# Optimization experiments

Measured on AMD Instinct MI355X. Metric: run time of the kernel, lower is better.

The kernel has to match this reference:

```python
import jax, jax.numpy as jnp
import numpy as np

N_NODES = 100_000
N_EDGES = 1_600_000
DIM_IN = 256
ADD_TO_EDGE_SCORE = 0.5  # PyG EdgePooling default


def setup_inputs() -> dict:
    key = jax.random.key(0)
    k1, k2, k3 = jax.random.split(key, 3)
    x = jax.random.normal(k1, (N_NODES, DIM_IN), dtype=jnp.float32)
    edge_index = jax.random.randint(k2, (2, N_EDGES), 0, N_NODES, dtype=jnp.int32)
    batch = jnp.zeros((N_NODES,), dtype=jnp.int32)  # single graph
    W = jax.random.normal(k3, (2 * DIM_IN, 1), dtype=jnp.float32) / np.sqrt(2.0 * DIM_IN)
    b = jnp.zeros((1,), dtype=jnp.float32)
    return {"x": x, "edge_index": edge_index, "batch": batch, "W": W, "b": b}


def _segment_softmax(scores, seg, num_segments):
    m = jax.ops.segment_max(scores, seg, num_segments=num_segments)
    ex = jnp.exp(scores - m[seg])
    s = jax.ops.segment_sum(ex, seg, num_segments=num_segments)
    return ex / s[seg]


def _greedy_matching(rank, src, dst, num_nodes):
    """Maximal matching equivalent to sequential greedy over edges sorted by
    ascending rank (rank = position in descending-score argsort, a strict total
    order). Implemented as parallel locally-dominant matching rounds."""
    big = jnp.iinfo(jnp.int32).max

    def cond(state):
        alive, matched, chosen = state
        return jnp.any(alive)

    def body(state):
        alive, matched, chosen = state
        r = jnp.where(alive, rank, big)
        node_min = jnp.full((num_nodes,), big, dtype=jnp.int32)
        node_min = node_min.at[src].min(r)
        node_min = node_min.at[dst].min(r)
        # an alive edge is picked if it dominates all alive edges at both endpoints
        pick = alive & (rank == node_min[src]) & (rank == node_min[dst])
        matched = matched.at[jnp.where(pick, src, num_nodes)].set(True, mode='drop')
        matched = matched.at[jnp.where(pick, dst, num_nodes)].set(True, mode='drop')
        chosen = chosen | pick
        alive = alive & ~matched[src] & ~matched[dst]
        return alive, matched, chosen

    alive0 = jnp.ones_like(rank, dtype=bool)
    matched0 = jnp.zeros((num_nodes,), dtype=bool)
    chosen0 = jnp.zeros_like(alive0)
    _, matched, chosen = jax.lax.while_loop(cond, body, (alive0, matched0, chosen0))
    return chosen, matched


def reference(x, edge_index, batch, W, b):
    num_nodes, feat = x.shape
    num_edges = edge_index.shape[1]
    src, dst = edge_index[0], edge_index[1]

    # Linear([x_src || x_dst]) split to avoid materializing [E, 2F]
    s_src = x @ W[:feat, 0]   # [N]
    s_dst = x @ W[feat:, 0]   # [N]
    raw = s_src[src] + s_dst[dst] + b[0]            # [E]
    # dropout is identity in eval mode
    e = _segment_softmax(raw, dst, num_nodes) + ADD_TO_EDGE_SCORE  # [E]

    # rank: position of each edge in descending-score order
    order = jnp.argsort(-e)
    rank = jnp.zeros((num_edges,), dtype=jnp.int32).at[order].set(
        jnp.arange(num_edges, dtype=jnp.int32))

    chosen, matched = _greedy_matching(rank, src, dst, num_nodes)

    # cluster id of each chosen edge = its position among chosen edges in score order
    chosen_sorted = chosen[order]
    cid_sorted = jnp.cumsum(chosen_sorted.astype(jnp.int32)) - 1
    cid = jnp.zeros((num_edges,), dtype=jnp.int32).at[order].set(cid_sorted)
    num_matched = jnp.sum(chosen.astype(jnp.int32))

    # node -> cluster assignment; unmatched nodes get trailing singleton clusters
    cluster = jnp.zeros((num_nodes,), dtype=jnp.int32)
    cluster = cluster.at[jnp.where(chosen, src, num_nodes)].set(cid, mode='drop')
    cluster = cluster.at[jnp.where(chosen, dst, num_nodes)].set(cid, mode='drop')
    unm = num_matched + jnp.cumsum((~matched).astype(jnp.int32)) - 1
    cluster = jnp.where(matched, cluster, unm)
    num_clusters = num_matched + jnp.sum((~matched).astype(jnp.int32))

    # per-cluster score: chosen-edge scores for merged pairs, 1.0 for singletons
    new_edge_score = jnp.ones((num_nodes,), dtype=x.dtype)
    new_edge_score = new_edge_score.at[jnp.where(chosen, cid, num_nodes)].set(e, mode='drop')

    # scatter-merge node features (rows >= num_clusters are zero padding)
    new_x = jax.ops.segment_sum(x, cluster, num_segments=num_nodes)
    new_x = new_x * new_edge_score[:, None]

    new_edge_index = cluster[edge_index]  # remapped edges (coalesce/dedup omitted)
    new_batch = jnp.zeros((num_nodes,), dtype=batch.dtype).at[cluster].set(batch)

    return new_x, new_edge_index, new_batch, num_clusters
```

## Files before the change

kernel.cpp:

```cpp
#include <hip/hip_runtime.h>

typedef unsigned int u32;
typedef unsigned long long u64;
typedef unsigned char u8;

static constexpr int SORTN = 65536;
static constexpr int STILE = 2048;
static constexpr int NR    = 12;
static constexpr int NHEAVY= 3;
static constexpr int NXCD  = 8;

__device__ __forceinline__ u32 xccid() {
  u32 x;
  asm volatile("s_getreg_b32 %0, hwreg(HW_REG_XCC_ID)" : "=s"(x));
  return x & (NXCD - 1);
}

__device__ __forceinline__ void wmin64(u64* p, u64 v) {
  __hip_atomic_fetch_min(p, v, __ATOMIC_RELAXED, __HIP_MEMORY_SCOPE_WORKGROUP);
}
__device__ __forceinline__ void wmax32(u32* p, u32 v) {
  __hip_atomic_fetch_max(p, v, __ATOMIC_RELAXED, __HIP_MEMORY_SCOPE_WORKGROUP);
}
__device__ __forceinline__ void waddf64(double* p, double v) {
  __hip_atomic_fetch_add(p, v, __ATOMIC_RELAXED, __HIP_MEMORY_SCOPE_WORKGROUP);
}

__device__ __forceinline__ u32 ordf(float f) {
  u32 u = __float_as_uint(f);
  return (u & 0x80000000u) ? ~u : (u | 0x80000000u);
}
__device__ __forceinline__ float inv_ordf(u32 m) {
  return __uint_as_float((m & 0x80000000u) ? (m ^ 0x80000000u) : ~m);
}

__global__ __launch_bounds__(256)
void k_init(u32* m_ord, u32* m8, double* ssum, double* ss8, u8* matched,
            u64* node_min, u64* nm8, float* scoreC, ulonglong2* sortbuf,
            u32* fcnt, u32* scalars, int N, int E) {
  int i = blockIdx.x * blockDim.x + threadIdx.x;
  if (i < N) { m_ord[i] = 0u; ssum[i] = 0.0; matched[i] = 0; scoreC[i] = 1.0f; }
  if (i < 2 * N) node_min[i] = ~0ull;
  if (i < NXCD * N) { nm8[i] = ~0ull; m8[i] = 0u; ss8[i] = 0.0; }
  if (i < SORTN) sortbuf[i] = make_ulonglong2(~0ull, ~0ull);
  if (i < 256)   fcnt[i] = 0u;
  if (i < 16)    scalars[i] = 0u;
  if (i == 0)    fcnt[0] = (u32)E;
}

__global__ __launch_bounds__(256)
void k_dots(const float4* __restrict__ x4, const float4* __restrict__ W4,
            float* __restrict__ s_src, float* __restrict__ s_dst, int N) {
  int gt = blockIdx.x * blockDim.x + threadIdx.x;
  int w = gt >> 6, lane = gt & 63;
  if (w >= N) return;
  float4 xa = x4[(size_t)w * 64 + lane];
  float4 wa = W4[lane];
  float4 wb = W4[64 + lane];
  float pa = xa.x*wa.x + xa.y*wa.y + xa.z*wa.z + xa.w*wa.w;
  float pb = xa.x*wb.x + xa.y*wb.y + xa.z*wb.z + xa.w*wb.w;
  #pragma unroll
  for (int m = 32; m >= 1; m >>= 1) {
    pa += __shfl_xor(pa, m);
    pb += __shfl_xor(pb, m);
  }
  if (lane == 0) { s_src[w] = pa; s_dst[w] = pb; }
}

__global__ __launch_bounds__(256)
void k_max8(const int* __restrict__ src, const int* __restrict__ dst,
            const float* __restrict__ s_src, const float* __restrict__ s_dst,
            const float* __restrict__ bvec, u32* m8, int N, int E) {
  int e = blockIdx.x * blockDim.x + threadIdx.x;
  if (e >= E) return;
  u32* mW = m8 + (size_t)xccid() * N;
  int d = dst[e];
  float r = s_src[src[e]] + s_dst[d] + bvec[0];
  wmax32(&mW[d], ordf(r));
}

__global__ __launch_bounds__(256)
void k_maxmerge(const u32* __restrict__ m8, u32* __restrict__ m_ord, int N) {
  int v = blockIdx.x * 256 + threadIdx.x;
  if (v >= N) return;
  u32 m = 0u;
  #pragma unroll
  for (int x = 0; x < NXCD; x++) {
    u32 t = m8[(size_t)x * N + v];
    m = (t > m) ? t : m;
  }
  m_ord[v] = m;
}

__global__ __launch_bounds__(256)
void k_expsum8(const int* __restrict__ src, const int* __restrict__ dst,
               const float* __restrict__ s_src, const float* __restrict__ s_dst,
               const float* __restrict__ bvec, const u32* __restrict__ m_ord,
               double* ss8, int N, int E) {
  int e = blockIdx.x * blockDim.x + threadIdx.x;
  if (e >= E) return;
  double* sW = ss8 + (size_t)xccid() * N;
  int d = dst[e];
  float r = s_src[src[e]] + s_dst[d] + bvec[0];
  float ex = expf(r - inv_ordf(m_ord[d]));
  waddf64(&sW[d], (double)ex);
}

__global__ __launch_bounds__(256)
void k_ssmerge(const double* __restrict__ ss8, double* __restrict__ ssum, int N) {
  int v = blockIdx.x * 256 + threadIdx.x;
  if (v >= N) return;
  double s = 0.0;
  #pragma unroll
  for (int x = 0; x < NXCD; x++) s += ss8[(size_t)x * N + v];
  ssum[v] = s;
}

__global__ __launch_bounds__(256)
void k_scorekey(const int* __restrict__ src, const int* __restrict__ dst,
                const float* __restrict__ s_src, const float* __restrict__ s_dst,
                const float* __restrict__ bvec, const u32* __restrict__ m_ord,
                const double* __restrict__ ssum,
                ulonglong2* __restrict__ front0, u64* nm8, int N, int E) {
  int e = blockIdx.x * blockDim.x + threadIdx.x;
  if (e >= E) return;
  u64* nmW = nm8 + (size_t)xccid() * N;
  int s = src[e], d = dst[e];
  float r = s_src[s] + s_dst[d] + bvec[0];
  float ex = expf(r - inv_ordf(m_ord[d]));
  float es = ex / (float)ssum[d] + 0.5f;
  u64 key = ((u64)(~ordf(es)) << 32) | (u32)e;
  u64 sd  = ((u64)(u32)s << 32) | (u32)d;
  front0[e] = make_ulonglong2(key, sd);
  wmin64(&nmW[s], key);
  if (d != s) wmin64(&nmW[d], key);
}

__global__ __launch_bounds__(256)
void k_merge(u64* nm8, u64* __restrict__ nmOut, int N) {
  int v = blockIdx.x * 256 + threadIdx.x;
  if (v >= N) return;
  u64 m = ~0ull;
  #pragma unroll
  for (int x = 0; x < NXCD; x++) {
    size_t idx = (size_t)x * N + v;
    u64 t = nm8[idx];
    if (t != ~0ull) { nm8[idx] = ~0ull; m = (t < m) ? t : m; }
  }
  nmOut[v] = m;
}

template<int R>
__global__ __launch_bounds__(256)
void k_mmin_h(const ulonglong2* __restrict__ fin, const u32* __restrict__ cntp,
              const u8* __restrict__ matched, u64* nm8, int N) {
  u32 cnt = *cntp;
  u64* nmW = nm8 + (size_t)xccid() * N;
  u32 nth = gridDim.x * 256;
  for (u32 i = blockIdx.x * 256 + threadIdx.x; i < cnt; i += nth) {
    ulonglong2 t = fin[i];
    int s = (int)(t.y >> 32), d = (int)(u32)t.y;
    if (matched[s] | matched[d]) continue;
    wmin64(&nmW[s], t.x);
    if (d != s) wmin64(&nmW[d], t.x);
  }
}

template<int R>
__global__ __launch_bounds__(256)
void k_mmin_l(const ulonglong2* __restrict__ fin, const u32* __restrict__ cntp,
              const u8* __restrict__ matched, u64* nm) {
  u32 cnt = *cntp;
  u32 nth = gridDim.x * 256;
  for (u32 i = blockIdx.x * 256 + threadIdx.x; i < cnt; i += nth) {
    ulonglong2 t = fin[i];
    int s = (int)(t.y >> 32), d = (int)(u32)t.y;
    if (matched[s] | matched[d]) continue;
    atomicMin(&nm[s], t.x);
    if (d != s) atomicMin(&nm[d], t.x);
  }
}

template<int R>
__global__ __launch_bounds__(256)
void k_mpick(const ulonglong2* __restrict__ fin, const u32* __restrict__ cntp,
             const u64* __restrict__ nm, u64* nmNext, u8* matched,
             ulonglong2* fout, u32* cntOut, ulonglong2* sortbuf, u32* scalars) {
  __shared__ u32 wb[4];
  __shared__ u32 bbase;
  u32 cnt = *cntp;
  int tx = threadIdx.x, lane = tx & 63, wid = tx >> 6;
  for (u32 base = blockIdx.x * 256; base < cnt; base += gridDim.x * 256) {
    u32 gid = base + tx;
    ulonglong2 t = make_ulonglong2(0ull, 0ull);
    int s = 0, d = 0;
    bool pk = false, surv = false;
    if (gid < cnt) {
      t = fin[gid];
      s = (int)(t.y >> 32); d = (int)(u32)t.y;
      if (!(matched[s] | matched[d])) {
        pk = (nm[s] == t.x) && (nm[d] == t.x);
        surv = !pk;
      }
    }
    u64 pm = __ballot(pk);
    if (pm) {
      u32 pre = (u32)__popcll(pm & ((1ull << lane) - 1ull));
      int ldr = __ffsll((long long)pm) - 1;
      u32 pb = 0;
      if (lane == ldr) pb = atomicAdd(&scalars[0], (u32)__popcll(pm));
      pb = __shfl(pb, ldr);
      if (pk) { matched[s] = 1; matched[d] = 1; sortbuf[pb + pre] = t; }
    }
    u64 sm = __ballot(surv);
    if (lane == 0) wb[wid] = (u32)__popcll(sm);
    __syncthreads();
    if (tx == 0) {
      u32 tt = wb[0] + wb[1] + wb[2] + wb[3];
      bbase = tt ? atomicAdd(cntOut, tt) : 0u;
    }
    __syncthreads();
    if (surv) {
      u32 woff = 0;
      for (int w = 0; w < wid; w++) woff += wb[w];
      u32 pre = (u32)__popcll(sm & ((1ull << lane) - 1ull));
      fout[bbase + woff + pre] = t;
      nmNext[s] = ~0ull;
      if (d != s) nmNext[d] = ~0ull;
    }
    __syncthreads();
  }
}

__global__ __launch_bounds__(1024)
void k_mfinish(ulonglong2* fA, ulonglong2* fB, u8* matched, u64* nm,
               ulonglong2* sortbuf, const u32* __restrict__ cntp, u32* scalars) {
  __shared__ u32 sh_cnt;
  u32 cnt = *cntp;
  int tx = threadIdx.x;
  ulonglong2* fin = fA; ulonglong2* fout = fB;
  while (cnt > 0) {
    for (u32 i = tx; i < cnt; i += 1024) {
      u64 p = fin[i].y;
      nm[p >> 32] = ~0ull; nm[(u32)p] = ~0ull;
    }
    if (tx == 0) sh_cnt = 0;
    __syncthreads();
    for (u32 i = tx; i < cnt; i += 1024) {
      ulonglong2 t = fin[i];
      int s = (int)(t.y >> 32), d = (int)(u32)t.y;
      if (matched[s] | matched[d]) continue;
      wmin64(&nm[s], t.x);
      if (d != s) wmin64(&nm[d], t.x);
    }
    __syncthreads();
    for (u32 i = tx; i < cnt; i += 1024) {
      ulonglong2 t = fin[i];
      int s = (int)(t.y >> 32), d = (int)(u32)t.y;
      if (matched[s] | matched[d]) continue;
      u64 a = __hip_atomic_fetch_add(&nm[s], 0ull, __ATOMIC_RELAXED,
                                     __HIP_MEMORY_SCOPE_WORKGROUP);
      u64 b = (d == s) ? a
            : __hip_atomic_fetch_add(&nm[d], 0ull, __ATOMIC_RELAXED,
                                     __HIP_MEMORY_SCOPE_WORKGROUP);
      if (a == t.x && b == t.x) {
        matched[s] = 1; matched[d] = 1;
        u32 o = atomicAdd(&scalars[0], 1u);
        sortbuf[o] = t;
      } else {
        u32 o = atomicAdd(&sh_cnt, 1u);
        fout[o] = t;
      }
    }
    __syncthreads();
    cnt = sh_cnt;
    ulonglong2* tmp = fin; fin = fout; fout = tmp;
    __syncthreads();
  }
}

__global__ __launch_bounds__(256)
void k_sort1(ulonglong2* buf) {
  __shared__ ulonglong2 t[STILE];
  const int base = blockIdx.x * STILE;
  for (int i = threadIdx.x; i < STILE; i += 256) t[i] = buf[base + i];
  __syncthreads();
  for (int k = 2; k <= STILE; k <<= 1) {
    for (int j = k >> 1; j > 0; j >>= 1) {
      for (int i = threadIdx.x; i < STILE; i += 256) {
        int p = i ^ j;
        if (p > i) {
          bool dir = (((base + i) & k) == 0);
          ulonglong2 a = t[i], c = t[p];
          if ((a.x > c.x) == dir) { t[i] = c; t[p] = a; }
        }
      }
      __syncthreads();
    }
  }
  for (int i = threadIdx.x; i < STILE; i += 256) buf[base + i] = t[i];
}

__global__ __launch_bounds__(256)
void k_gpass(ulonglong2* buf, int j, int k) {
  int i = blockIdx.x * 256 + threadIdx.x;
  int p = i ^ j;
  if (p > i && p < SORTN) {
    bool dir = ((i & k) == 0);
    ulonglong2 a = buf[i], c = buf[p];
    if ((a.x > c.x) == dir) { buf[i] = c; buf[p] = a; }
  }
}

__global__ __launch_bounds__(256)
void k_sortl(ulonglong2* buf, int k) {
  __shared__ ulonglong2 t[STILE];
  const int base = blockIdx.x * STILE;
  const bool dir = ((base & k) == 0);
  for (int i = threadIdx.x; i < STILE; i += 256) t[i] = buf[base + i];
  __syncthreads();
  for (int j = STILE >> 1; j > 0; j >>= 1) {
    for (int i = threadIdx.x; i < STILE; i += 256) {
      int p = i ^ j;
      if (p > i) {
        ulonglong2 a = t[i], c = t[p];
        if ((a.x > c.x) == dir) { t[i] = c; t[p] = a; }
      }
    }
    __syncthreads();
  }
  for (int i = threadIdx.x; i < STILE; i += 256) buf[base + i] = t[i];
}

__global__ __launch_bounds__(256)
void k_assign(const ulonglong2* __restrict__ buf,
              int* cluster, int* memA, int* memB, float* scoreC,
              const u32* __restrict__ scalars) {
  int i = blockIdx.x * blockDim.x + threadIdx.x;
  if (i >= (int)scalars[0]) return;
  ulonglong2 t = buf[i];
  int s = (int)(t.y >> 32), d = (int)(u32)t.y;
  cluster[s] = i; cluster[d] = i;
  scoreC[i] = inv_ordf(~(u32)(t.x >> 32));
  memA[i] = s;
  memB[i] = (s == d) ? -1 : d;
}

__global__ __launch_bounds__(256)
void k_scan1(const u8* __restrict__ matched, u32* partials, int N) {
  __shared__ u32 sh[256];
  int b = blockIdx.x, tx = threadIdx.x;
  int v0 = b * 1024 + tx * 4;
  u32 c = 0;
  #pragma unroll
  for (int q = 0; q < 4; q++) { int v = v0 + q; if (v < N && !matched[v]) c++; }
  sh[tx] = c; __syncthreads();
  for (int s = 128; s > 0; s >>= 1) { if (tx < s) sh[tx] += sh[tx + s]; __syncthreads(); }
  if (tx == 0) partials[b] = sh[0];
}

__global__ void k_scan2(const u32* partials, u32* partials2, u32* scalars, int NB) {
  if (blockIdx.x == 0 && threadIdx.x == 0) {
    u32 run = 0;
    for (int i = 0; i < NB; i++) { partials2[i] = run; run += partials[i]; }
    scalars[1] = run;
    scalars[2] = scalars[0] + run;
  }
}

__global__ __launch_bounds__(256)
void k_scan3(const u8* __restrict__ matched, const u32* __restrict__ partials2,
             const u32* __restrict__ scalars, int* cluster, int* memA, int* memB, int N) {
  __shared__ u32 sh[256];
  int b = blockIdx.x, tx = threadIdx.x;
  int v0 = b * 1024 + tx * 4;
  u32 f[4]; u32 c = 0;
  #pragma unroll
  for (int q = 0; q < 4; q++) { int v = v0 + q; f[q] = (v < N && !matched[v]); c += f[q]; }
  sh[tx] = c; __syncthreads();
  for (int s = 1; s < 256; s <<= 1) {
    u32 x = sh[tx];
    u32 y = (tx >= s) ? sh[tx - s] : 0;
    __syncthreads();
    sh[tx] = x + y;
    __syncthreads();
  }
  u32 base = scalars[0] + partials2[b] + (sh[tx] - c);
  #pragma unroll
  for (int q = 0; q < 4; q++) {
    if (f[q]) {
      int v = v0 + q;
      int cc = (int)base++;
      cluster[v] = cc; memA[cc] = v; memB[cc] = -1;
    }
  }
}

__global__ __launch_bounds__(256)
void k_newx(const float4* __restrict__ x4, const int* __restrict__ memA,
            const int* __restrict__ memB, const float* __restrict__ scoreC,
            const u32* __restrict__ scalars, float4* __restrict__ out4, int N) {
  int gt = blockIdx.x * blockDim.x + threadIdx.x;
  int w = gt >> 6, lane = gt & 63;
  if (w >= N) return;
  int nc = (int)scalars[2];
  float4 o;
  if (w < nc) {
    int a = memA[w], b = memB[w];
    float s = scoreC[w];
    float4 va = x4[(size_t)a * 64 + lane];
    float ox = va.x, oy = va.y, oz = va.z, ow = va.w;
    if (b >= 0) {
      float4 vb = x4[(size_t)b * 64 + lane];
      ox += vb.x; oy += vb.y; oz += vb.z; ow += vb.w;
    }
    o = make_float4(ox * s, oy * s, oz * s, ow * s);
  } else {
    o = make_float4(0.f, 0.f, 0.f, 0.f);
  }
  out4[(size_t)w * 64 + lane] = o;
}

__global__ __launch_bounds__(256)
void k_remap(const int* __restrict__ ei, const int* __restrict__ cluster,
             float* __restrict__ outE, int twoE) {
  int i = blockIdx.x * blockDim.x + threadIdx.x;
  if (i < twoE) outE[i] = (float)cluster[ei[i]];
}

__global__ __launch_bounds__(256)
void k_tail(float* __restrict__ outB, const u32* __restrict__ scalars, int N) {
  int i = blockIdx.x * blockDim.x + threadIdx.x;
  if (i < N) outB[i] = 0.0f;
  if (i == 0) outB[N] = (float)scalars[2];
}

template<int R>
static void launch_rounds(ulonglong2* frontA, ulonglong2* frontB, u64* nm8,
                          u64* node_min, u8* matched, ulonglong2* sortbuf,
                          u32* fcnt, u32* scalars, int N, int NB_E,
                          hipStream_t stream) {
  if constexpr (R < NR) {
    ulonglong2* fin  = (R & 1) ? frontB : frontA;
    ulonglong2* fout = (R & 1) ? frontA : frontB;
    u64* nm  = node_min + (size_t)(R & 1) * N;
    u64* nmN = node_min + (size_t)((R & 1) ^ 1) * N;
    int nbr = NB_E >> R; if (nbr < 256) nbr = 256;
    if constexpr (R == 0) {
    } else if constexpr (R < NHEAVY) {
      k_mmin_h<R><<<nbr, 256, 0, stream>>>(fin, fcnt + R, matched, nm8, N);
      k_merge<<<(N + 255) / 256, 256, 0, stream>>>(nm8, nm, N);
    } else {
      k_mmin_l<R><<<nbr, 256, 0, stream>>>(fin, fcnt + R, matched, nm);
    }
    k_mpick<R><<<nbr, 256, 0, stream>>>(fin, fcnt + R, nm, nmN, matched,
                                        fout, fcnt + R + 1, sortbuf, scalars);
    launch_rounds<R + 1>(frontA, frontB, nm8, node_min, matched, sortbuf,
                         fcnt, scalars, N, NB_E, stream);
  }
}

extern "C" void kernel_launch(void* const* d_in, const int* in_sizes, int n_in,
                              void* d_out, int out_size, void* d_ws, size_t ws_size,
                              hipStream_t stream) {
  const float* x    = (const float*)d_in[0];
  const int*   ei   = (const int*)d_in[1];
  const float* W    = (const float*)d_in[3];
  const float* bvec = (const float*)d_in[4];
  int N = in_sizes[2];
  int E = in_sizes[1] / 2;

  char* p = (char*)d_ws;
  auto alloc = [&](size_t bytes) { char* r = p; p += (bytes + 255) & ~(size_t)255; return r; };
  float*      s_src    = (float*)alloc((size_t)N * 4);
  float*      s_dst    = (float*)alloc((size_t)N * 4);
  u32*        m_ord    = (u32*)alloc((size_t)N * 4);
  u32*        m8       = (u32*)alloc((size_t)NXCD * N * 4);
  double*     ssum     = (double*)alloc((size_t)N * 8);
  double*     ss8      = (double*)alloc((size_t)NXCD * N * 8);
  ulonglong2* frontA   = (ulonglong2*)alloc((size_t)E * 16);
  ulonglong2* frontB   = (ulonglong2*)alloc((size_t)E * 16);
  u8*         matched  = (u8*)alloc((size_t)N);
  u64*        node_min = (u64*)alloc((size_t)2 * N * 8);
  u64*        nm8      = (u64*)alloc((size_t)NXCD * N * 8);
  ulonglong2* sortbuf  = (ulonglong2*)alloc((size_t)SORTN * 16);
  int*        cluster  = (int*)alloc((size_t)N * 4);
  int*        memA     = (int*)alloc((size_t)N * 4);
  int*        memB     = (int*)alloc((size_t)N * 4);
  float*      scoreC   = (float*)alloc((size_t)N * 4);
  u32*        fcnt     = (u32*)alloc(1024);
  u32*        partials = (u32*)alloc(4096);
  u32*        partials2= (u32*)alloc(4096);
  u32*        scalars  = (u32*)alloc(256);
  (void)ws_size; (void)out_size; (void)n_in;

  const int* srcp = ei;
  const int* dstp = ei + E;
  float* out  = (float*)d_out;
  float* outX = out;
  float* outE = out + (size_t)N * 256;
  float* outB = outE + (size_t)2 * E;

  int NB_E = (E + 255) / 256;
  int cover = NXCD * N; if (cover < SORTN) cover = SORTN;
  k_init<<<(cover + 255) / 256, 256, 0, stream>>>(m_ord, m8, ssum, ss8, matched,
                                                  node_min, nm8, scoreC, sortbuf,
                                                  fcnt, scalars, N, E);
  k_dots<<<((size_t)N * 64 + 255) / 256, 256, 0, stream>>>(
      (const float4*)x, (const float4*)W, s_src, s_dst, N);
  k_max8<<<NB_E, 256, 0, stream>>>(srcp, dstp, s_src, s_dst, bvec, m8, N, E);
  k_maxmerge<<<(N + 255) / 256, 256, 0, stream>>>(m8, m_ord, N);
  k_expsum8<<<NB_E, 256, 0, stream>>>(srcp, dstp, s_src, s_dst, bvec, m_ord, ss8, N, E);
  k_ssmerge<<<(N + 255) / 256, 256, 0, stream>>>(ss8, ssum, N);
  k_scorekey<<<NB_E, 256, 0, stream>>>(srcp, dstp, s_src, s_dst, bvec, m_ord, ssum,
                                       frontA, nm8, N, E);
  k_merge<<<(N + 255) / 256, 256, 0, stream>>>(nm8, node_min, N);

  launch_rounds<0>(frontA, frontB, nm8, node_min, matched, sortbuf, fcnt, scalars,
                   N, NB_E, stream);
  k_mfinish<<<1, 1024, 0, stream>>>(frontA, frontB, matched, node_min,
                                    sortbuf, fcnt + NR, scalars);

  k_sort1<<<SORTN / STILE, 256, 0, stream>>>(sortbuf);
  for (int k = STILE << 1; k <= SORTN; k <<= 1) {
    for (int j = k >> 1; j >= STILE; j >>= 1)
      k_gpass<<<SORTN / 256, 256, 0, stream>>>(sortbuf, j, k);
    k_sortl<<<SORTN / STILE, 256, 0, stream>>>(sortbuf, k);
  }

  k_assign<<<SORTN / 256, 256, 0, stream>>>(sortbuf, cluster, memA, memB, scoreC, scalars);
  int NB = (N + 1023) / 1024;
  k_scan1<<<NB, 256, 0, stream>>>(matched, partials, N);
  k_scan2<<<1, 64, 0, stream>>>(partials, partials2, scalars, NB);
  k_scan3<<<NB, 256, 0, stream>>>(matched, partials2, scalars, cluster, memA, memB, N);

  k_newx<<<((size_t)N * 64 + 255) / 256, 256, 0, stream>>>(
      (const float4*)x, memA, memB, scoreC, scalars, (float4*)outX, N);
  k_remap<<<(2 * E + 255) / 256, 256, 0, stream>>>(ei, cluster, outE, 2 * E);
  k_tail<<<(N + 255) / 256, 256, 0, stream>>>(outB, scalars, N);
}
```

Measured before the change: 1.596 ms.

## Cache raw edge scores, extend grid rounds, double-buffer finisher node-min, fuse tail

Stores each edge's raw score once in k_max8, so the exp-sum and score-key kernels no longer re-gather s_src/s_dst. Raises the number of grid-wide matching rounds from 12 to 28, with a smaller minimum grid of 64 blocks, so less work falls to the single-block finisher. The finisher now double-buffers node_min and resets only the surviving edges' entries, which removes its separate reset pass. The tail kernel is merged into k_remap to save a launch, at the cost of an extra E-sized float buffer and more kernel launches for the added rounds.

```diff
diff --git a/kernel.cpp b/kernel.cpp
--- a/kernel.cpp
+++ b/kernel.cpp
@@ -6,7 +6,7 @@
 
 static constexpr int SORTN = 65536;
 static constexpr int STILE = 2048;
-static constexpr int NR    = 12;
+static constexpr int NR    = 28;
 static constexpr int NHEAVY= 3;
 static constexpr int NXCD  = 8;
 
@@ -70,12 +70,14 @@
 __global__ __launch_bounds__(256)
 void k_max8(const int* __restrict__ src, const int* __restrict__ dst,
             const float* __restrict__ s_src, const float* __restrict__ s_dst,
-            const float* __restrict__ bvec, u32* m8, int N, int E) {
+            const float* __restrict__ bvec, u32* m8, float* __restrict__ raw,
+            int N, int E) {
   int e = blockIdx.x * blockDim.x + threadIdx.x;
   if (e >= E) return;
   u32* mW = m8 + (size_t)xccid() * N;
   int d = dst[e];
   float r = s_src[src[e]] + s_dst[d] + bvec[0];
+  raw[e] = r;
   wmax32(&mW[d], ordf(r));
 }
 
@@ -93,16 +95,13 @@
 }
 
 __global__ __launch_bounds__(256)
-void k_expsum8(const int* __restrict__ src, const int* __restrict__ dst,
-               const float* __restrict__ s_src, const float* __restrict__ s_dst,
-               const float* __restrict__ bvec, const u32* __restrict__ m_ord,
-               double* ss8, int N, int E) {
+void k_expsum8(const int* __restrict__ dst, const float* __restrict__ raw,
+               const u32* __restrict__ m_ord, double* ss8, int N, int E) {
   int e = blockIdx.x * blockDim.x + threadIdx.x;
   if (e >= E) return;
   double* sW = ss8 + (size_t)xccid() * N;
   int d = dst[e];
-  float r = s_src[src[e]] + s_dst[d] + bvec[0];
-  float ex = expf(r - inv_ordf(m_ord[d]));
+  float ex = expf(raw[e] - inv_ordf(m_ord[d]));
   waddf64(&sW[d], (double)ex);
 }
 
@@ -118,16 +117,14 @@
 
 __global__ __launch_bounds__(256)
 void k_scorekey(const int* __restrict__ src, const int* __restrict__ dst,
-                const float* __restrict__ s_src, const float* __restrict__ s_dst,
-                const float* __restrict__ bvec, const u32* __restrict__ m_ord,
+                const float* __restrict__ raw, const u32* __restrict__ m_ord,
                 const double* __restrict__ ssum,
                 ulonglong2* __restrict__ front0, u64* nm8, int N, int E) {
   int e = blockIdx.x * blockDim.x + threadIdx.x;
   if (e >= E) return;
   u64* nmW = nm8 + (size_t)xccid() * N;
   int s = src[e], d = dst[e];
-  float r = s_src[s] + s_dst[d] + bvec[0];
-  float ex = expf(r - inv_ordf(m_ord[d]));
+  float ex = expf(raw[e] - inv_ordf(m_ord[d]));
   float es = ex / (float)ssum[d] + 0.5f;
   u64 key = ((u64)(~ordf(es)) << 32) | (u32)e;
   u64 sd  = ((u64)(u32)s << 32) | (u32)d;
@@ -233,35 +230,32 @@
 }
 
 __global__ __launch_bounds__(1024)
-void k_mfinish(ulonglong2* fA, ulonglong2* fB, u8* matched, u64* nm,
+void k_mfinish(ulonglong2* fA, ulonglong2* fB, u8* matched, u64* nmA, u64* nmB,
                ulonglong2* sortbuf, const u32* __restrict__ cntp, u32* scalars) {
   __shared__ u32 sh_cnt;
   u32 cnt = *cntp;
   int tx = threadIdx.x;
   ulonglong2* fin = fA; ulonglong2* fout = fB;
+  u64* nmCur = nmA; u64* nmNxt = nmB;
   while (cnt > 0) {
-    for (u32 i = tx; i < cnt; i += 1024) {
-      u64 p = fin[i].y;
-      nm[p >> 32] = ~0ull; nm[(u32)p] = ~0ull;
-    }
     if (tx == 0) sh_cnt = 0;
     __syncthreads();
     for (u32 i = tx; i < cnt; i += 1024) {
       ulonglong2 t = fin[i];
       int s = (int)(t.y >> 32), d = (int)(u32)t.y;
       if (matched[s] | matched[d]) continue;
-      wmin64(&nm[s], t.x);
-      if (d != s) wmin64(&nm[d], t.x);
+      wmin64(&nmCur[s], t.x);
+      if (d != s) wmin64(&nmCur[d], t.x);
     }
     __syncthreads();
     for (u32 i = tx; i < cnt; i += 1024) {
       ulonglong2 t = fin[i];
       int s = (int)(t.y >> 32), d = (int)(u32)t.y;
       if (matched[s] | matched[d]) continue;
-      u64 a = __hip_atomic_fetch_add(&nm[s], 0ull, __ATOMIC_RELAXED,
+      u64 a = __hip_atomic_fetch_add(&nmCur[s], 0ull, __ATOMIC_RELAXED,
                                      __HIP_MEMORY_SCOPE_WORKGROUP);
       u64 b = (d == s) ? a
-            : __hip_atomic_fetch_add(&nm[d], 0ull, __ATOMIC_RELAXED,
+            : __hip_atomic_fetch_add(&nmCur[d], 0ull, __ATOMIC_RELAXED,
                                      __HIP_MEMORY_SCOPE_WORKGROUP);
       if (a == t.x && b == t.x) {
         matched[s] = 1; matched[d] = 1;
@@ -270,11 +264,14 @@
       } else {
         u32 o = atomicAdd(&sh_cnt, 1u);
         fout[o] = t;
+        nmNxt[s] = ~0ull;
+        if (d != s) nmNxt[d] = ~0ull;
       }
     }
     __syncthreads();
     cnt = sh_cnt;
-    ulonglong2* tmp = fin; fin = fout; fout = tmp;
+    ulonglong2* tf = fin; fin = fout; fout = tf;
+    u64* tn = nmCur; nmCur = nmNxt; nmNxt = tn;
     __syncthreads();
   }
 }
@@ -423,16 +420,13 @@
 
 __global__ __launch_bounds__(256)
 void k_remap(const int* __restrict__ ei, const int* __restrict__ cluster,
-             float* __restrict__ outE, int twoE) {
+             float* __restrict__ outE, float* __restrict__ outB,
+             const u32* __restrict__ scalars, int twoE, int N) {
   int i = blockIdx.x * blockDim.x + threadIdx.x;
   if (i < twoE) outE[i] = (float)cluster[ei[i]];
-}
-
-__global__ __launch_bounds__(256)
-void k_tail(float* __restrict__ outB, const u32* __restrict__ scalars, int N) {
-  int i = blockIdx.x * blockDim.x + threadIdx.x;
-  if (i < N) outB[i] = 0.0f;
-  if (i == 0) outB[N] = (float)scalars[2];
+  int j = i - twoE;
+  if (j >= 0 && j < N) outB[j] = 0.0f;
+  if (j == N) outB[N] = (float)scalars[2];
 }
 
 template<int R>
@@ -445,7 +439,7 @@
     ulonglong2* fout = (R & 1) ? frontA : frontB;
     u64* nm  = node_min + (size_t)(R & 1) * N;
     u64* nmN = node_min + (size_t)((R & 1) ^ 1) * N;
-    int nbr = NB_E >> R; if (nbr < 256) nbr = 256;
+    int nbr = (R < 30) ? (NB_E >> R) : 0; if (nbr < 64) nbr = 64;
     if constexpr (R == 0) {
     } else if constexpr (R < NHEAVY) {
       k_mmin_h<R><<<nbr, 256, 0, stream>>>(fin, fcnt + R, matched, nm8, N);
@@ -478,6 +472,7 @@
   u32*        m8       = (u32*)alloc((size_t)NXCD * N * 4);
   double*     ssum     = (double*)alloc((size_t)N * 8);
   double*     ss8      = (double*)alloc((size_t)NXCD * N * 8);
+  float*      raw      = (float*)alloc((size_t)E * 4);
   ulonglong2* frontA   = (ulonglong2*)alloc((size_t)E * 16);
   ulonglong2* frontB   = (ulonglong2*)alloc((size_t)E * 16);
   u8*         matched  = (u8*)alloc((size_t)N);
@@ -508,17 +503,18 @@
                                                   fcnt, scalars, N, E);
   k_dots<<<((size_t)N * 64 + 255) / 256, 256, 0, stream>>>(
       (const float4*)x, (const float4*)W, s_src, s_dst, N);
-  k_max8<<<NB_E, 256, 0, stream>>>(srcp, dstp, s_src, s_dst, bvec, m8, N, E);
+  k_max8<<<NB_E, 256, 0, stream>>>(srcp, dstp, s_src, s_dst, bvec, m8, raw, N, E);
   k_maxmerge<<<(N + 255) / 256, 256, 0, stream>>>(m8, m_ord, N);
-  k_expsum8<<<NB_E, 256, 0, stream>>>(srcp, dstp, s_src, s_dst, bvec, m_ord, ss8, N, E);
+  k_expsum8<<<NB_E, 256, 0, stream>>>(dstp, raw, m_ord, ss8, N, E);
   k_ssmerge<<<(N + 255) / 256, 256, 0, stream>>>(ss8, ssum, N);
-  k_scorekey<<<NB_E, 256, 0, stream>>>(srcp, dstp, s_src, s_dst, bvec, m_ord, ssum,
+  k_scorekey<<<NB_E, 256, 0, stream>>>(srcp, dstp, raw, m_ord, ssum,
                                        frontA, nm8, N, E);
   k_merge<<<(N + 255) / 256, 256, 0, stream>>>(nm8, node_min, N);
 
   launch_rounds<0>(frontA, frontB, nm8, node_min, matched, sortbuf, fcnt, scalars,
                    N, NB_E, stream);
-  k_mfinish<<<1, 1024, 0, stream>>>(frontA, frontB, matched, node_min,
+  k_mfinish<<<1, 1024, 0, stream>>>(frontA, frontB, matched,
+                                    node_min, node_min + N,
                                     sortbuf, fcnt + NR, scalars);
 
   k_sort1<<<SORTN / STILE, 256, 0, stream>>>(sortbuf);
@@ -536,6 +532,6 @@
 
   k_newx<<<((size_t)N * 64 + 255) / 256, 256, 0, stream>>>(
       (const float4*)x, memA, memB, scoreC, scalars, (float4*)outX, N);
-  k_remap<<<(2 * E + 255) / 256, 256, 0, stream>>>(ei, cluster, outE, 2 * E);
-  k_tail<<<(N + 255) / 256, 256, 0, stream>>>(outB, scalars, N);
-}
+  k_remap<<<(2 * E + N + 1 + 255) / 256, 256, 0, stream>>>(
+      ei, cluster, outE, outB, scalars, 2 * E, N);
+}
```

New measurement: 1.470 ms. 1.09x faster.
